# Optimization experiments

Hardware: AMD Instinct MI355X
Metric: run time of the kernel (lower is better)

## Reference

```python
import jax, jax.numpy as jnp
import numpy as np

S, I, H = 4096, 1024, 1024  # seq_len, input_size, hidden_size


def setup_inputs() -> dict:
    key = jax.random.key(0)
    ks = jax.random.split(key, 5)
    scale = 1.0 / np.sqrt(H + I)  # nn.Linear default U(-1/sqrt(fan_in), 1/sqrt(fan_in))
    def lin_w(k):
        return jax.random.uniform(k, (4 * H, H + I), jnp.float32, -scale, scale)
    kb1, kb2 = jax.random.split(ks[4])
    return {
        "inputs": jax.random.normal(ks[0], (S, I), jnp.float32),
        # rows stacked as [f; i; g; o] gates, columns as [h | x] (matches cat([h, x]))
        "fwd_W": lin_w(ks[1]),
        "fwd_b": jax.random.uniform(kb1, (4 * H,), jnp.float32, -scale, scale),
        "bwd_W": lin_w(ks[2]),
        "bwd_b": jax.random.uniform(kb2, (4 * H,), jnp.float32, -scale, scale),
    }


def _run_direction(inputs, W, b, reverse):
    # W: (4H, H+I); split into recurrent part (acts on h) and input part (acts on x)
    Wh = W[:, :H]            # (4H, H)
    Wx = W[:, H:]            # (4H, I)
    # Precompute input contribution for all timesteps in one big GEMM: (S, 4H)
    x_proj = inputs @ Wx.T + b

    def step(carry, xp):
        h, c = carry
        z = Wh @ h + xp                          # (4H,)
        f, i, g, o = jnp.split(z, 4)
        c_t = jax.nn.sigmoid(f) * c + jax.nn.sigmoid(i) * jnp.tanh(g)
        h_t = jax.nn.sigmoid(o) * jnp.tanh(c_t)
        return (h_t, c_t), h_t

    h0 = jnp.zeros((H,), inputs.dtype)
    (h_final, _), hs = jax.lax.scan(step, (h0, h0), x_proj, reverse=reverse)
    # scan with reverse=True emits stacked outputs in original (forward) order
    return hs, h_final


def reference(inputs, fwd_W, fwd_b, bwd_W, bwd_b):
    f_hs, f_h = _run_direction(inputs, fwd_W, fwd_b, reverse=False)
    b_hs, b_h = _run_direction(inputs, bwd_W, bwd_b, reverse=True)
    all_hidden = jnp.concatenate([f_hs, b_hs], axis=-1)   # (S, 2H)
    final_h = jnp.concatenate([f_h, b_h], axis=-1)        # (2H,)
    return (all_hidden, final_h)
```

## Files before the change

kernel.cpp:

```cpp
#include <hip/hip_runtime.h>
#include <hip/hip_bf16.h>
#include <cstdint>
#include <cstddef>


typedef __attribute__((ext_vector_type(8))) short short8;
typedef __attribute__((ext_vector_type(4))) short short4v;
typedef __attribute__((ext_vector_type(4))) float float4v;
typedef unsigned long long ull;

__device__ __forceinline__ float bf2f(unsigned short u) {
    return __uint_as_float(((unsigned int)u) << 16);
}
__device__ __forceinline__ unsigned short f2bf(float f) {
    __hip_bfloat16 h = __float2bfloat16(f);
    return *reinterpret_cast<unsigned short*>(&h);
}
__device__ __forceinline__ float sigm(float x) {
    return 1.f / (1.f + __expf(-x));
}
__device__ __forceinline__ float tanh_fast(float x) {
    return 1.f - 2.f / (__expf(2.f * x) + 1.f);
}

__global__ __launch_bounds__(256)
void xproj_gemm(const float* __restrict__ inp,
                const float* __restrict__ fw,
                const float* __restrict__ fb,
                const float* __restrict__ bw,
                const float* __restrict__ bb,
                float* __restrict__ xp)
{
    const int d  = blockIdx.z;
    const float* W = d ? bw : fw;
    const float* B = d ? bb : fb;
    const int t0 = blockIdx.y * 128;
    const int n0 = blockIdx.x * 128;

    __shared__ __align__(16) short Ash[128 * 32];
    __shared__ __align__(16) short Bsh[128 * 32];

    const int tid  = threadIdx.x;
    const int lane = tid & 63;
    const int wave = tid >> 6;
    const int wm = (wave & 1) * 64;
    const int wn = (wave >> 1) * 64;
    const int quad = lane >> 4;
    const int l15  = lane & 15;

    float4v acc[4][4];
    float4v zero4 = {0.f, 0.f, 0.f, 0.f};
#pragma unroll
    for (int mi = 0; mi < 4; mi++)
#pragma unroll
        for (int ni = 0; ni < 4; ni++) acc[mi][ni] = zero4;

    for (int k0 = 0; k0 < 1024; k0 += 32) {
#pragma unroll
        for (int s = 0; s < 4; s++) {
            int c   = tid + s * 256;
            int row = c >> 3;
            int ko  = (c & 7) * 4;
            float4v va = *(const float4v*)&inp[(size_t)(t0 + row) * 1024 + k0 + ko];
            float4v vb = *(const float4v*)&W[(size_t)(n0 + row) * 2048 + 1024 + k0 + ko];
            short4v sa, sb;
#pragma unroll
            for (int e = 0; e < 4; e++) {
                sa[e] = (short)f2bf(va[e]);
                sb[e] = (short)f2bf(vb[e]);
            }
            *(short4v*)&Ash[row * 32 + ko] = sa;
            *(short4v*)&Bsh[row * 32 + ko] = sb;
        }
        __syncthreads();

        short8 af[4], bfr[4];
#pragma unroll
        for (int mi = 0; mi < 4; mi++)
            af[mi] = *(const short8*)&Ash[(wm + mi * 16 + l15) * 32 + quad * 8];
#pragma unroll
        for (int ni = 0; ni < 4; ni++)
            bfr[ni] = *(const short8*)&Bsh[(wn + ni * 16 + l15) * 32 + quad * 8];

#pragma unroll
        for (int mi = 0; mi < 4; mi++)
#pragma unroll
            for (int ni = 0; ni < 4; ni++)
                acc[mi][ni] = __builtin_amdgcn_mfma_f32_16x16x32_bf16(
                    af[mi], bfr[ni], acc[mi][ni], 0, 0, 0);
        __syncthreads();
    }

#pragma unroll
    for (int ni = 0; ni < 4; ni++) {
        int gc = n0 + wn + ni * 16 + l15;
        float bias = B[gc];
#pragma unroll
        for (int mi = 0; mi < 4; mi++) {
#pragma unroll
            for (int r = 0; r < 4; r++) {
                int gr = t0 + wm + mi * 16 + quad * 4 + r;
                xp[((size_t)d * 4096 + gr) * 4096 + gc] = acc[mi][ni][r] + bias;
            }
        }
    }
}

template <int FUSED>
__global__ __launch_bounds__(512, 2)
void lstm_rec(const float* __restrict__ fw,
              const float* __restrict__ bw,
              const float* __restrict__ fb,
              const float* __restrict__ bb,
              const float* __restrict__ inp,
              const float* __restrict__ xp,
              ull* __restrict__ hq,
              float* __restrict__ out)
{
    const int dir  = blockIdx.x & 1;
    const int slot = blockIdx.x >> 1;
    const int u0   = slot * 16;
    const int T    = threadIdx.x;
    const int rl   = T & 63;
    const int gate = rl >> 4;
    const int ul   = rl & 15;
    const int chunk = T >> 6;
    const int j    = gate * 1024 + u0 + ul;
    const float* W = dir ? bw : fw;

    __shared__ __align__(16) float hsh[1024];
    __shared__ __align__(16) float xsh[1024];
    __shared__ float xvs[2][64];
    __shared__ float psum[2][64 * 9];

    float w[128];
    {
        const float* wr = W + (size_t)j * 2048 + chunk * 128;
#pragma unroll
        for (int i = 0; i < 32; i++)
            *(float4v*)&w[4 * i] = *(const float4v*)&wr[4 * i];
    }

    unsigned int w2[64];
    float bj4[4];
    if (FUSED) {
        const float* wr2 = W + (size_t)j * 2048 + 1024 + chunk * 128;
#pragma unroll
        for (int i = 0; i < 32; i++) {
            float4v v = *(const float4v*)&wr2[4 * i];
            w2[2 * i]     = (unsigned int)f2bf(v[0]) | ((unsigned int)f2bf(v[1]) << 16);
            w2[2 * i + 1] = (unsigned int)f2bf(v[2]) | ((unsigned int)f2bf(v[3]) << 16);
        }
        if (T < 16) {
#pragma unroll
            for (int g = 0; g < 4; g++)
                bj4[g] = (dir ? bb : fb)[g * 1024 + u0 + T];
        }
    }

    ull* hqd = hq + dir * 2048;
    float c = 0.f;

    for (int t = 0; t < 4096; t++) {
        const int tr  = dir ? (4095 - t) : t;
        const int par = t & 1;

        float xv = 0.f;
        float2 iv;
        if (FUSED) {
            iv = ((const float2*)&inp[(size_t)tr * 1024])[T];
        } else if (T < 64) {
            xv = xp[((size_t)dir * 4096 + tr) * 4096 + j];
        }

        {
            ull* q0 = &hqd[par * 1024 + 2 * T];
            ull w0 = __hip_atomic_load(q0, __ATOMIC_RELAXED, __HIP_MEMORY_SCOPE_AGENT);
            ull w1 = __hip_atomic_load(q0 + 1, __ATOMIC_RELAXED, __HIP_MEMORY_SCOPE_AGENT);
            while ((unsigned)(w0 >> 32) != (unsigned)t)
                w0 = __hip_atomic_load(q0, __ATOMIC_RELAXED, __HIP_MEMORY_SCOPE_AGENT);
            while ((unsigned)(w1 >> 32) != (unsigned)t)
                w1 = __hip_atomic_load(q0 + 1, __ATOMIC_RELAXED, __HIP_MEMORY_SCOPE_AGENT);
            hsh[2 * T]     = __uint_as_float((unsigned)w0);
            hsh[2 * T + 1] = __uint_as_float((unsigned)w1);
        }
        if (FUSED) {
            xsh[2 * T]     = iv.x;
            xsh[2 * T + 1] = iv.y;
        } else if (T < 64) {
            xvs[par][T] = xv;
        }
        __syncthreads();

        float a0 = 0.f, a1 = 0.f, a2 = 0.f, a3 = 0.f;
        const float4v* h4 = (const float4v*)&hsh[chunk * 128];
#pragma unroll
        for (int i = 0; i < 32; i++) {
            float4v hv = h4[i];
            a0 = __builtin_fmaf(w[4 * i + 0], hv.x, a0);
            a1 = __builtin_fmaf(w[4 * i + 1], hv.y, a1);
            a2 = __builtin_fmaf(w[4 * i + 2], hv.z, a2);
            a3 = __builtin_fmaf(w[4 * i + 3], hv.w, a3);
        }
        if (FUSED) {
            const float* xs = &xsh[chunk * 128];
#pragma unroll
            for (int i = 0; i < 64; i++) {
                unsigned int dv = w2[i];
                a0 = __builtin_fmaf(bf2f((unsigned short)(dv & 0xffffu)),
                                    xs[2 * i], a0);
                a1 = __builtin_fmaf(bf2f((unsigned short)(dv >> 16)),
                                    xs[2 * i + 1], a1);
            }
        }
        psum[par][rl * 9 + chunk] = (a0 + a1) + (a2 + a3);
        __syncthreads();

        if (T < 16) {
            float z[4];
#pragma unroll
            for (int g = 0; g < 4; g++) {
                int row = g * 16 + T;
                float s = FUSED ? bj4[g] : xvs[par][row];
                const float* pp = &psum[par][row * 9];
#pragma unroll
                for (int cc = 0; cc < 8; cc++) s += pp[cc];
                z[g] = s;
            }
            c = sigm(z[0]) * c + sigm(z[1]) * tanh_fast(z[2]);
            float hv = sigm(z[3]) * tanh_fast(c);
            out[(size_t)tr * 2048 + dir * 1024 + u0 + T] = hv;
            if (t == 4095)
                out[(size_t)4096 * 2048 + dir * 1024 + u0 + T] = hv;
            __hip_atomic_store(&hqd[((t + 1) & 1) * 1024 + u0 + T],
                               ((ull)(unsigned)(t + 1) << 32) | __float_as_uint(hv),
                               __ATOMIC_RELAXED, __HIP_MEMORY_SCOPE_AGENT);
        }
    }
}

extern "C" void kernel_launch(void* const* d_in, const int* in_sizes, int n_in,
                              void* d_out, int out_size, void* d_ws, size_t ws_size,
                              hipStream_t stream)
{
    const float* inp = (const float*)d_in[0];
    const float* fw  = (const float*)d_in[1];
    const float* fb  = (const float*)d_in[2];
    const float* bw  = (const float*)d_in[3];
    const float* bb  = (const float*)d_in[4];

    char* ws = (char*)d_ws;
    ull* hq   = (ull*)ws;
    float* xp = (float*)(ws + 32768);

    const size_t XP_BYTES = 2ull * 4096 * 4096 * 4;
    const int have_xp = (ws_size >= 32768 + XP_BYTES);

    hipMemsetAsync(ws, 0, 32768, stream);

    float* outp = (float*)d_out;
    if (have_xp) {
        dim3 gg(32, 32, 2);
        xproj_gemm<<<gg, 256, 0, stream>>>(inp, fw, fb, bw, bb, xp);
        lstm_rec<0><<<dim3(128), 512, 0, stream>>>(fw, bw, fb, bb, inp, xp,
                                                   hq, outp);
    } else {
        lstm_rec<1><<<dim3(128), 512, 0, stream>>>(fw, bw, fb, bb, inp, nullptr,
                                                   hq, outp);
    }
}
```

Measured before the change: 9.593 ms.

## Spread LSTM recurrence over 256 blocks with replicated hidden-state mailboxes

Halves the hidden units per block (8 instead of 16) and launches 256 blocks so each thread holds fewer recurrent weights and does a shorter dot product. The hidden-state exchange buffer is replicated 8 times, with each producer writing all copies, to spread polling traffic across memory. It also removes one block barrier by relying on wavefront-local LDS ordering, adds s_sleep in the spin loop, and computes gate activations in parallel via shuffles. The cost is more blocks in the global step-to-step synchronisation and extra atomic stores per step.

```diff
diff --git a/kernel.cpp b/kernel.cpp
--- a/kernel.cpp
+++ b/kernel.cpp
@@ -106,7 +106,7 @@
     }
 }
 
-template <int FUSED>
+template <int FUSED, int NREP>
 __global__ __launch_bounds__(512, 2)
 void lstm_rec(const float* __restrict__ fw,
               const float* __restrict__ bw,
@@ -114,51 +114,47 @@
               const float* __restrict__ bb,
               const float* __restrict__ inp,
               const float* __restrict__ xp,
-              ull* __restrict__ hq,
+              ull* hq,
               float* __restrict__ out)
 {
     const int dir  = blockIdx.x & 1;
     const int slot = blockIdx.x >> 1;
-    const int u0   = slot * 16;
+    const int u0   = slot * 8;
+    const int rep  = slot & (NREP - 1);
     const int T    = threadIdx.x;
-    const int rl   = T & 63;
-    const int gate = rl >> 4;
-    const int ul   = rl & 15;
-    const int chunk = T >> 6;
-    const int j    = gate * 1024 + u0 + ul;
+    const int rl   = T & 31;
+    const int ch   = T >> 5;
+    const int gate = rl >> 3;
+    const int un   = rl & 7;
+    const int j    = gate * 1024 + u0 + un;
     const float* W = dir ? bw : fw;
 
     __shared__ __align__(16) float hsh[1024];
     __shared__ __align__(16) float xsh[1024];
-    __shared__ float xvs[2][64];
-    __shared__ float psum[2][64 * 9];
-
-    float w[128];
+    __shared__ float psum[2][32 * 17];
+
+    float w[64];
     {
-        const float* wr = W + (size_t)j * 2048 + chunk * 128;
-#pragma unroll
-        for (int i = 0; i < 32; i++)
+        const float* wr = W + (size_t)j * 2048 + ch * 64;
+#pragma unroll
+        for (int i = 0; i < 16; i++)
             *(float4v*)&w[4 * i] = *(const float4v*)&wr[4 * i];
     }
 
-    unsigned int w2[64];
-    float bj4[4];
+    unsigned int w2[32];
+    float bj = 0.f;
     if (FUSED) {
-        const float* wr2 = W + (size_t)j * 2048 + 1024 + chunk * 128;
-#pragma unroll
-        for (int i = 0; i < 32; i++) {
+        const float* wr2 = W + (size_t)j * 2048 + 1024 + ch * 64;
+#pragma unroll
+        for (int i = 0; i < 16; i++) {
             float4v v = *(const float4v*)&wr2[4 * i];
             w2[2 * i]     = (unsigned int)f2bf(v[0]) | ((unsigned int)f2bf(v[1]) << 16);
             w2[2 * i + 1] = (unsigned int)f2bf(v[2]) | ((unsigned int)f2bf(v[3]) << 16);
         }
-        if (T < 16) {
-#pragma unroll
-            for (int g = 0; g < 4; g++)
-                bj4[g] = (dir ? bb : fb)[g * 1024 + u0 + T];
-        }
-    }
-
-    ull* hqd = hq + dir * 2048;
+        if (T < 32) bj = (dir ? bb : fb)[j];
+    }
+
+    ull* hqd = hq + (size_t)(rep * 2 + dir) * 2048;
     float c = 0.f;
 
     for (int t = 0; t < 4096; t++) {
@@ -169,33 +165,32 @@
         float2 iv;
         if (FUSED) {
             iv = ((const float2*)&inp[(size_t)tr * 1024])[T];
-        } else if (T < 64) {
+        } else if (T < 32) {
             xv = xp[((size_t)dir * 4096 + tr) * 4096 + j];
         }
 
         {
-            ull* q0 = &hqd[par * 1024 + 2 * T];
-            ull w0 = __hip_atomic_load(q0, __ATOMIC_RELAXED, __HIP_MEMORY_SCOPE_AGENT);
-            ull w1 = __hip_atomic_load(q0 + 1, __ATOMIC_RELAXED, __HIP_MEMORY_SCOPE_AGENT);
-            while ((unsigned)(w0 >> 32) != (unsigned)t)
-                w0 = __hip_atomic_load(q0, __ATOMIC_RELAXED, __HIP_MEMORY_SCOPE_AGENT);
-            while ((unsigned)(w1 >> 32) != (unsigned)t)
-                w1 = __hip_atomic_load(q0 + 1, __ATOMIC_RELAXED, __HIP_MEMORY_SCOPE_AGENT);
+            ull* q = &hqd[par * 1024 + 2 * T];
+            ull w0 = __hip_atomic_load(q, __ATOMIC_RELAXED, __HIP_MEMORY_SCOPE_AGENT);
+            ull w1 = __hip_atomic_load(q + 1, __ATOMIC_RELAXED, __HIP_MEMORY_SCOPE_AGENT);
+            while ((unsigned)(w0 >> 32) != (unsigned)t ||
+                   (unsigned)(w1 >> 32) != (unsigned)t) {
+                __builtin_amdgcn_s_sleep(1);
+                w0 = __hip_atomic_load(q, __ATOMIC_RELAXED, __HIP_MEMORY_SCOPE_AGENT);
+                w1 = __hip_atomic_load(q + 1, __ATOMIC_RELAXED, __HIP_MEMORY_SCOPE_AGENT);
+            }
             hsh[2 * T]     = __uint_as_float((unsigned)w0);
             hsh[2 * T + 1] = __uint_as_float((unsigned)w1);
         }
         if (FUSED) {
             xsh[2 * T]     = iv.x;
             xsh[2 * T + 1] = iv.y;
-        } else if (T < 64) {
-            xvs[par][T] = xv;
-        }
-        __syncthreads();
+        }
 
         float a0 = 0.f, a1 = 0.f, a2 = 0.f, a3 = 0.f;
-        const float4v* h4 = (const float4v*)&hsh[chunk * 128];
-#pragma unroll
-        for (int i = 0; i < 32; i++) {
+        const float4v* h4 = (const float4v*)&hsh[ch * 64];
+#pragma unroll
+        for (int i = 0; i < 16; i++) {
             float4v hv = h4[i];
             a0 = __builtin_fmaf(w[4 * i + 0], hv.x, a0);
             a1 = __builtin_fmaf(w[4 * i + 1], hv.y, a1);
@@ -203,9 +198,9 @@
             a3 = __builtin_fmaf(w[4 * i + 3], hv.w, a3);
         }
         if (FUSED) {
-            const float* xs = &xsh[chunk * 128];
-#pragma unroll
-            for (int i = 0; i < 64; i++) {
+            const float* xs = &xsh[ch * 64];
+#pragma unroll
+            for (int i = 0; i < 32; i++) {
                 unsigned int dv = w2[i];
                 a0 = __builtin_fmaf(bf2f((unsigned short)(dv & 0xffffu)),
                                     xs[2 * i], a0);
@@ -213,28 +208,34 @@
                                     xs[2 * i + 1], a1);
             }
         }
-        psum[par][rl * 9 + chunk] = (a0 + a1) + (a2 + a3);
+        psum[par][rl * 17 + ch] = (a0 + a1) + (a2 + a3);
         __syncthreads();
 
-        if (T < 16) {
-            float z[4];
-#pragma unroll
-            for (int g = 0; g < 4; g++) {
-                int row = g * 16 + T;
-                float s = FUSED ? bj4[g] : xvs[par][row];
-                const float* pp = &psum[par][row * 9];
-#pragma unroll
-                for (int cc = 0; cc < 8; cc++) s += pp[cc];
-                z[g] = s;
-            }
-            c = sigm(z[0]) * c + sigm(z[1]) * tanh_fast(z[2]);
-            float hv = sigm(z[3]) * tanh_fast(c);
-            out[(size_t)tr * 2048 + dir * 1024 + u0 + T] = hv;
-            if (t == 4095)
-                out[(size_t)4096 * 2048 + dir * 1024 + u0 + T] = hv;
-            __hip_atomic_store(&hqd[((t + 1) & 1) * 1024 + u0 + T],
-                               ((ull)(unsigned)(t + 1) << 32) | __float_as_uint(hv),
-                               __ATOMIC_RELAXED, __HIP_MEMORY_SCOPE_AGENT);
+        if (T < 64) {
+            float v = 0.f;
+            if (T < 32) {
+                float s = FUSED ? bj : xv;
+                const float* pp = &psum[par][T * 17];
+#pragma unroll
+                for (int cc = 0; cc < 16; cc++) s += pp[cc];
+                v = (T >= 16 && T < 24) ? tanh_fast(s) : sigm(s);
+            }
+            float iv2 = __shfl(v, un + 8, 64);
+            float gv  = __shfl(v, un + 16, 64);
+            float ov  = __shfl(v, un + 24, 64);
+            if (T < 8) {
+                c = v * c + iv2 * gv;
+                float hv = ov * tanh_fast(c);
+                out[(size_t)tr * 2048 + dir * 1024 + u0 + T] = hv;
+                if (t == 4095)
+                    out[(size_t)4096 * 2048 + dir * 1024 + u0 + T] = hv;
+                ull pw = ((ull)(unsigned)(t + 1) << 32) | __float_as_uint(hv);
+#pragma unroll
+                for (int r2 = 0; r2 < NREP; r2++)
+                    __hip_atomic_store(
+                        &hq[(size_t)(r2 * 2 + dir) * 2048 + ((t + 1) & 1) * 1024 + u0 + T],
+                        pw, __ATOMIC_RELAXED, __HIP_MEMORY_SCOPE_AGENT);
+            }
         }
     }
 }
@@ -250,22 +251,25 @@
     const float* bb  = (const float*)d_in[4];
 
     char* ws = (char*)d_ws;
-    ull* hq   = (ull*)ws;
-    float* xp = (float*)(ws + 32768);
-
+    ull* hq = (ull*)ws;
+    const size_t HQ8  = 8 * 32768;
+    float* xp = (float*)(ws + HQ8);
     const size_t XP_BYTES = 2ull * 4096 * 4096 * 4;
-    const int have_xp = (ws_size >= 32768 + XP_BYTES);
-
-    hipMemsetAsync(ws, 0, 32768, stream);
 
     float* outp = (float*)d_out;
-    if (have_xp) {
+    if (ws_size >= HQ8 + XP_BYTES) {
+        hipMemsetAsync(ws, 0, HQ8, stream);
         dim3 gg(32, 32, 2);
         xproj_gemm<<<gg, 256, 0, stream>>>(inp, fw, fb, bw, bb, xp);
-        lstm_rec<0><<<dim3(128), 512, 0, stream>>>(fw, bw, fb, bb, inp, xp,
-                                                   hq, outp);
+        lstm_rec<0, 8><<<dim3(256), 512, 0, stream>>>(fw, bw, fb, bb, inp, xp,
+                                                      hq, outp);
+    } else if (ws_size >= HQ8) {
+        hipMemsetAsync(ws, 0, HQ8, stream);
+        lstm_rec<1, 8><<<dim3(256), 512, 0, stream>>>(fw, bw, fb, bb, inp, nullptr,
+                                                      hq, outp);
     } else {
-        lstm_rec<1><<<dim3(128), 512, 0, stream>>>(fw, bw, fb, bb, inp, nullptr,
-                                                   hq, outp);
-    }
-}
+        hipMemsetAsync(ws, 0, 32768, stream);
+        lstm_rec<1, 1><<<dim3(256), 512, 0, stream>>>(fw, bw, fb, bb, inp, nullptr,
+                                                      hq, outp);
+    }
+}
```

Result: slower. 9.957 ms (+3.8%).
